# Optimization experiments

Hardware: AMD Instinct MI355X
Metric: run time of the kernel (lower is better)

## Reference

```python
import jax, jax.numpy as jnp
import numpy as np


def setup_inputs() -> dict:
    key = jax.random.key(0)
    ks = jax.random.split(key, 8)
    B, T, U = 4, 400, 80
    De, Dd, V = 512, 512, 1024
    F = De + Dd  # in_features = 1024
    s = lambda k, shape: jax.random.normal(k, shape, dtype=jnp.float32) * 0.05
    return {
        "encoder_output": jax.random.normal(ks[0], (B, T, De), dtype=jnp.float32),
        "decoder_output": jax.random.normal(ks[1], (B, U, Dd), dtype=jnp.float32),
        "W_enc": s(ks[2], (F, De)),
        "b_enc": s(ks[3], (F,)),
        "W_dec": s(ks[4], (F, Dd)),
        "b_dec": s(ks[5], (F,)),
        "W_fc": s(ks[6], (V, F)),
        "b_fc": s(ks[7], (V,)),
    }


def reference(encoder_output, decoder_output, W_enc, b_enc, W_dec, b_dec, W_fc, b_fc):
    # fc_enc / fc_dec projections: (B,T,F) and (B,U,F)
    enc = jnp.einsum("btd,fd->btf", encoder_output, W_enc) + b_enc
    dec = jnp.einsum("bud,fd->buf", decoder_output, W_dec) + b_dec
    # broadcast-add -> (B,T,U,F)
    combined = enc[:, :, None, :] + dec[:, None, :, :]
    # fc: tanh then linear -> (B,T,U,V)
    vocab_logits = jnp.einsum("btuf,vf->btuv", jnp.tanh(combined), W_fc) + b_fc
    # HAT branch: blank prob via sigmoid of logit 0
    blk_logit = vocab_logits[..., :1]
    log_blk = jax.nn.log_sigmoid(blk_logit)          # log(sigmoid)
    log_not_blk = jax.nn.log_sigmoid(-blk_logit)     # log(1 - sigmoid)
    vocab_log_probs = log_not_blk + jax.nn.log_softmax(vocab_logits[..., 1:], axis=-1)
    return jnp.concatenate([log_blk, vocab_log_probs], axis=-1)
```

## Files before the change

kernel.cpp:

```cpp
#include <hip/hip_runtime.h>
#include <hip/hip_bf16.h>
#include <cstdint>
#include <cstddef>

typedef short bf16x8 __attribute__((ext_vector_type(8)));
typedef float f32x4 __attribute__((ext_vector_type(4)));

static __device__ __forceinline__ unsigned short f2bf(float f) {
    union { float f; uint32_t u; } c; c.f = f;
    uint32_t r = c.u + 0x7FFFu + ((c.u >> 16) & 1u);
    return (unsigned short)(r >> 16);
}
static __device__ __forceinline__ float bf2f_lo(uint32_t w) {
    union { uint32_t u; float f; } c; c.u = w << 16; return c.f;
}
static __device__ __forceinline__ float bf2f_hi(uint32_t w) {
    union { uint32_t u; float f; } c; c.u = w & 0xffff0000u; return c.f;
}
static __device__ __forceinline__ float fast_tanh(float x) {
    float e = __expf(2.0f * x);
    return 1.0f - 2.0f / (e + 1.0f);
}
static __device__ __forceinline__ float softplus_f(float x) {
    return fmaxf(x, 0.0f) + log1pf(__expf(-fabsf(x)));
}

#define GLOAD_LDS16(g, l) \
    __builtin_amdgcn_global_load_lds((const __attribute__((address_space(1))) void*)(g), \
                                     (__attribute__((address_space(3))) void*)(l), 16, 0, 0)

__global__ __launch_bounds__(256) void k_convert(
    const float* __restrict__ s0, const float* __restrict__ s1,
    const float* __restrict__ s2, const float* __restrict__ s3,
    const float* __restrict__ s4,
    unsigned short* __restrict__ d0, unsigned short* __restrict__ d1,
    unsigned short* __restrict__ d2, unsigned short* __restrict__ d3,
    unsigned short* __restrict__ d4,
    int n0, int n1, int n2, int n3, int n4)
{
    int i = blockIdx.x * 256 + threadIdx.x;
    int c0 = n0 >> 2, c1 = c0 + (n1 >> 2), c2 = c1 + (n2 >> 2),
        c3 = c2 + (n3 >> 2), c4 = c3 + (n4 >> 2);
    if (i >= c4) return;
    const float* s; unsigned short* d; int j;
    if (i < c0)      { s = s0; d = d0; j = i; }
    else if (i < c1) { s = s1; d = d1; j = i - c0; }
    else if (i < c2) { s = s2; d = d2; j = i - c1; }
    else if (i < c3) { s = s3; d = d3; j = i - c2; }
    else             { s = s4; d = d4; j = i - c3; }
    float4 v = reinterpret_cast<const float4*>(s)[j];
    ushort4 o;
    o.x = f2bf(v.x); o.y = f2bf(v.y); o.z = f2bf(v.z); o.w = f2bf(v.w);
    reinterpret_cast<ushort4*>(d)[j] = o;
}

__global__ __launch_bounds__(256) void k_proj(
    const unsigned short* __restrict__ A,
    const unsigned short* __restrict__ W,
    const float* __restrict__ bias,
    float* __restrict__ out)
{
    __shared__ unsigned short As[32 * 512];
    const int tid = threadIdx.x;
    const int m0 = blockIdx.x * 32;
    const int c0 = blockIdx.y * 128;
    {
        int row = tid >> 3;
        const unsigned short* src = A + (size_t)(m0 + row) * 512;
        unsigned int base = row * 1024;
        unsigned int sw = (row & 7) << 4;
        #pragma unroll
        for (int c = 0; c < 8; ++c) {
            int col = (tid & 7) * 8 + c * 64;
            bf16x8 v = *reinterpret_cast<const bf16x8*>(src + col);
            *reinterpret_cast<bf16x8*>(
                reinterpret_cast<char*>(As) + ((base + col * 2) ^ sw)) = v;
        }
    }
    __syncthreads();
    const int w = tid >> 6, l = tid & 63;
    const int lr = l & 15, lkb = (l >> 4) * 8;
    f32x4 acc[2][2] = {};
    const int colbase = c0 + w * 32;
    const unsigned short* Wb = W + (size_t)(colbase + lr) * 512 + lkb;
    const unsigned int sw = (lr & 7) << 4;
    for (int ks = 0; ks < 16; ++ks) {
        unsigned int kb = (ks * 32 + lkb) * 2;
        bf16x8 a0 = *reinterpret_cast<const bf16x8*>(
            reinterpret_cast<const char*>(As) + ((lr * 1024 + kb) ^ sw));
        bf16x8 a1 = *reinterpret_cast<const bf16x8*>(
            reinterpret_cast<const char*>(As) + (((16 + lr) * 1024 + kb) ^ sw));
        #pragma unroll
        for (int nf = 0; nf < 2; ++nf) {
            bf16x8 b = *reinterpret_cast<const bf16x8*>(Wb + nf * 16 * 512 + ks * 32);
            acc[0][nf] = __builtin_amdgcn_mfma_f32_16x16x32_bf16(a0, b, acc[0][nf], 0, 0, 0);
            acc[1][nf] = __builtin_amdgcn_mfma_f32_16x16x32_bf16(a1, b, acc[1][nf], 0, 0, 0);
        }
    }
    const int qr = (l >> 4) * 4;
    #pragma unroll
    for (int nf = 0; nf < 2; ++nf) {
        int col = colbase + nf * 16 + lr;
        float bv = bias[col];
        #pragma unroll
        for (int mf = 0; mf < 2; ++mf)
            #pragma unroll
            for (int r = 0; r < 4; ++r)
                out[(size_t)(m0 + mf * 16 + qr + r) * 1024 + col] = acc[mf][nf][r] + bv;
    }
}

__global__ __launch_bounds__(256) void k_tanhA(
    const float* __restrict__ enc_f,
    const float* __restrict__ dec_f,
    char* __restrict__ outb)
{
    const int NG = 128000 * 128;
    for (int g = blockIdx.x * 256 + threadIdx.x; g < NG; g += gridDim.x * 256) {
        int row = g >> 7, c8 = g & 127;
        int bt = row / 80;
        int u = row - bt * 80;
        int b = bt / 400;
        const float* ep = enc_f + (size_t)bt * 1024 + c8 * 8;
        const float* dp = dec_f + (size_t)(b * 80 + u) * 1024 + c8 * 8;
        float4 e0 = *(const float4*)ep, e1 = *(const float4*)(ep + 4);
        float4 f0 = *(const float4*)dp, f1 = *(const float4*)(dp + 4);
        uint4 pk;
        pk.x = (uint32_t)f2bf(fast_tanh(e0.x + f0.x)) | ((uint32_t)f2bf(fast_tanh(e0.y + f0.y)) << 16);
        pk.y = (uint32_t)f2bf(fast_tanh(e0.z + f0.z)) | ((uint32_t)f2bf(fast_tanh(e0.w + f0.w)) << 16);
        pk.z = (uint32_t)f2bf(fast_tanh(e1.x + f1.x)) | ((uint32_t)f2bf(fast_tanh(e1.y + f1.y)) << 16);
        pk.w = (uint32_t)f2bf(fast_tanh(e1.z + f1.z)) | ((uint32_t)f2bf(fast_tanh(e1.w + f1.w)) << 16);
        *(uint4*)(outb + (size_t)row * 4096 + c8 * 16) = pk;
    }
}

__global__ __launch_bounds__(512, 1) void k_gemm(
    const unsigned short* __restrict__ Wfc,
    const float* __restrict__ bfc,
    char* __restrict__ outb)
{
    extern __shared__ char smem[];
    const int tid = threadIdx.x;
    const int w = tid >> 6, l = tid & 63;
    const int lr = l & 15, q = l >> 4;
    const int wm = w >> 2, wn = w & 3;

    const int bid = (int)blockIdx.x;
    const int g = (bid & 7) * 250 + (bid >> 3);
    const size_t R0 = (size_t)(g >> 2) * 256;
    const int n0 = (g & 3) * 256;

    const unsigned kb0 = (unsigned)(((tid & 7) * 16) ^ (((tid >> 3) & 7) << 4));
    const int row0 = tid >> 3;
    const char* sA = outb + (R0 + row0) * 4096 + kb0;
    const char* sB = (const char*)Wfc + (size_t)(n0 + row0) * 2048 + kb0;

#define STAGE(dbuf, koff) do { \
    const char* _a = sA + (koff); \
    const char* _b = sB + (koff); \
    char* _d = smem + (dbuf) * 65536 + tid * 16; \
    GLOAD_LDS16(_a,          _d);          \
    GLOAD_LDS16(_a + 262144, _d + 8192);   \
    GLOAD_LDS16(_a + 524288, _d + 16384);  \
    GLOAD_LDS16(_a + 786432, _d + 24576);  \
    GLOAD_LDS16(_b,          _d + 32768);  \
    GLOAD_LDS16(_b + 131072, _d + 40960);  \
    GLOAD_LDS16(_b + 262144, _d + 49152);  \
    GLOAD_LDS16(_b + 393216, _d + 57344);  \
} while (0)

    const unsigned key = (unsigned)((lr & 7) << 4);
    const unsigned kx0 = (unsigned)(q * 16) ^ key;
    const unsigned kx1 = (unsigned)(q * 16 + 64) ^ key;
    const unsigned abase = (unsigned)((wm * 128 + lr) * 128);
    const unsigned bbase = (unsigned)(32768 + (wn * 64 + lr) * 128);

    f32x4 acc[8][4] = {};
    bf16x8 af[4][2], bf[4][2];

    STAGE(0, 0);
    asm volatile("s_waitcnt vmcnt(0)" ::: "memory");
    __builtin_amdgcn_s_barrier();
    __builtin_amdgcn_sched_barrier(0);

#define LDA(h) do { \
    _Pragma("unroll") \
    for (int mf = 0; mf < 4; ++mf) { \
        const char* _p = smem + cb + abase + (h) * 8192 + mf * 2048; \
        af[mf][0] = *(const bf16x8*)(_p + kx0); \
        af[mf][1] = *(const bf16x8*)(_p + kx1); \
    } } while (0)
#define LDB(gg) do { \
    _Pragma("unroll") \
    for (int j = 0; j < 2; ++j) { \
        const char* _p = smem + cb + bbase + ((gg) * 2 + j) * 2048; \
        bf[(gg) * 2 + j][0] = *(const bf16x8*)(_p + kx0); \
        bf[(gg) * 2 + j][1] = *(const bf16x8*)(_p + kx1); \
    } } while (0)
#define MFQ(h, gg) do { \
    __builtin_amdgcn_s_setprio(1); \
    _Pragma("unroll") \
    for (int j = 0; j < 2; ++j) \
        _Pragma("unroll") \
        for (int ks = 0; ks < 2; ++ks) \
            _Pragma("unroll") \
            for (int mf = 0; mf < 4; ++mf) \
                acc[(h) * 4 + mf][(gg) * 2 + j] = __builtin_amdgcn_mfma_f32_16x16x32_bf16( \
                    bf[(gg) * 2 + j][ks], af[mf][ks], acc[(h) * 4 + mf][(gg) * 2 + j], 0, 0, 0); \
    __builtin_amdgcn_s_setprio(0); \
} while (0)

    #pragma unroll 2
    for (int t = 0; t < 16; ++t) {
        const unsigned cb = (unsigned)(t & 1) * 65536;
        if (t + 1 < 16) STAGE((t & 1) ^ 1, (t + 1) * 128);
        LDA(0);
        LDB(0);
        __builtin_amdgcn_s_barrier();
        MFQ(0, 0);
        LDB(1);
        __builtin_amdgcn_s_barrier();
        MFQ(0, 1);
        LDA(1);
        __builtin_amdgcn_s_barrier();
        MFQ(1, 1);
        __builtin_amdgcn_s_barrier();
        MFQ(1, 0);
        asm volatile("s_waitcnt vmcnt(0)" ::: "memory");
        __builtin_amdgcn_s_barrier();
        __builtin_amdgcn_sched_barrier(0);
    }
#undef LDA
#undef LDB
#undef MFQ
#undef STAGE

    #pragma unroll
    for (int nf = 0; nf < 4; ++nf) {
        const int v = n0 + wn * 64 + nf * 16 + q * 4;
        float4 bv = *(const float4*)(bfc + v);
        #pragma unroll
        for (int mf8 = 0; mf8 < 8; ++mf8) {
            f32x4 a = acc[mf8][nf];
            uint2 pk;
            pk.x = (uint32_t)f2bf(a[0] + bv.x) | ((uint32_t)f2bf(a[1] + bv.y) << 16);
            pk.y = (uint32_t)f2bf(a[2] + bv.z) | ((uint32_t)f2bf(a[3] + bv.w) << 16);
            size_t m = R0 + (size_t)(wm * 128 + mf8 * 16 + lr);
            *(uint2*)(outb + m * 4096 + 2048 + (size_t)v * 2) = pk;
        }
    }
}

__global__ __launch_bounds__(256) void k_softmax(char* __restrict__ outb)
{
    const int row = blockIdx.x * 4 + (threadIdx.x >> 6);
    const int l = threadIdx.x & 63;
    const char* lp = outb + (size_t)row * 4096 + 2048 + l * 32;
    uint4 wa = *(const uint4*)lp;
    uint4 wb = *(const uint4*)(lp + 16);
    float v[16];
    uint32_t wd[8] = { wa.x, wa.y, wa.z, wa.w, wb.x, wb.y, wb.z, wb.w };
    #pragma unroll
    for (int i = 0; i < 8; ++i) { v[2*i] = bf2f_lo(wd[i]); v[2*i+1] = bf2f_hi(wd[i]); }

    float l0 = __shfl(v[0], 0);
    float m = (l == 0) ? -3.0e38f : v[0];
    #pragma unroll
    for (int i = 1; i < 16; ++i) m = fmaxf(m, v[i]);
    #pragma unroll
    for (int s = 1; s < 64; s <<= 1) m = fmaxf(m, __shfl_xor(m, s));
    float s = (l == 0) ? 0.0f : __expf(v[0] - m);
    #pragma unroll
    for (int i = 1; i < 16; ++i) s += __expf(v[i] - m);
    #pragma unroll
    for (int sh = 1; sh < 64; sh <<= 1) s += __shfl_xor(s, sh);

    float lse = m + __logf(s);
    float fin = -lse - softplus_f(l0);
    float f0v = -softplus_f(-l0);

    float* op = (float*)(outb + (size_t)row * 4096) + l * 16;
    #pragma unroll
    for (int c = 0; c < 4; ++c) {
        float4 o;
        o.x = v[4*c+0] + fin; o.y = v[4*c+1] + fin;
        o.z = v[4*c+2] + fin; o.w = v[4*c+3] + fin;
        if (l == 0 && c == 0) o.x = f0v;
        *(float4*)(op + 4*c) = o;
    }
}

extern "C" void kernel_launch(void* const* d_in, const int* in_sizes, int n_in,
                              void* d_out, int out_size, void* d_ws, size_t ws_size,
                              hipStream_t stream)
{
    const float* encoder = (const float*)d_in[0];
    const float* decoder = (const float*)d_in[1];
    const float* W_enc   = (const float*)d_in[2];
    const float* b_enc   = (const float*)d_in[3];
    const float* W_dec   = (const float*)d_in[4];
    const float* b_dec   = (const float*)d_in[5];
    const float* W_fc    = (const float*)d_in[6];
    const float* b_fc    = (const float*)d_in[7];
    char* outb = (char*)d_out;

    char* ws = (char*)d_ws;
    float*          enc_f  = (float*)(ws);
    float*          dec_f  = (float*)(ws + 6553600);
    unsigned short* Wfc_h  = (unsigned short*)(ws + 7864320);
    unsigned short* Wenc_h = (unsigned short*)(ws + 9961472);
    unsigned short* Wdec_h = (unsigned short*)(ws + 11010048);
    unsigned short* encI_h = (unsigned short*)(ws + 12058624);
    unsigned short* decI_h = (unsigned short*)(ws + 13697024);

    const int nEnc = 4 * 400 * 512, nDec = 4 * 80 * 512;
    const int nWe = 1024 * 512, nWd = 1024 * 512, nWf = 1024 * 1024;
    const int totalF4 = (nEnc + nDec + nWe + nWd + nWf) >> 2;
    k_convert<<<(totalF4 + 255) / 256, 256, 0, stream>>>(
        encoder, decoder, W_enc, W_dec, W_fc,
        encI_h, decI_h, Wenc_h, Wdec_h, Wfc_h,
        nEnc, nDec, nWe, nWd, nWf);

    k_proj<<<dim3(1600 / 32, 8), 256, 0, stream>>>(encI_h, Wenc_h, b_enc, enc_f);
    k_proj<<<dim3(320 / 32, 8), 256, 0, stream>>>(decI_h, Wdec_h, b_dec, dec_f);

    k_tanhA<<<4096, 256, 0, stream>>>(enc_f, dec_f, outb);

    const int GEMM_SMEM = 131072;
    hipFuncSetAttribute(reinterpret_cast<const void*>(k_gemm),
                        hipFuncAttributeMaxDynamicSharedMemorySize, GEMM_SMEM);
    k_gemm<<<2000, 512, GEMM_SMEM, stream>>>(Wfc_h, b_fc, outb);

    k_softmax<<<32000, 256, 0, stream>>>(outb);
}
```

Baseline: 697.4 us.

## Interleave global-to-LDS prefetch chunks across MFMA phases with deeper lookahead

```diff
diff --git a/kernel.cpp b/kernel.cpp
--- a/kernel.cpp
+++ b/kernel.cpp
@@ -154,11 +154,11 @@
     const int row0 = tid >> 3;
     const char* sA = outb + (R0 + row0) * 4096 + kb0;
     const char* sB = (const char*)Wfc + (size_t)(n0 + row0) * 2048 + kb0;
-
-#define STAGE(dbuf, koff) do { \
-    const char* _a = sA + (koff); \
-    const char* _b = sB + (koff); \
-    char* _d = smem + (dbuf) * 65536 + tid * 16; \
+    char* const dbase = smem + tid * 16;
+
+#define STG_ALL8(buf, T) do { \
+    const char* _a = sA + (T) * 128; const char* _b = sB + (T) * 128; \
+    char* _d = dbase + (buf); \
     GLOAD_LDS16(_a,          _d);          \
     GLOAD_LDS16(_a + 262144, _d + 8192);   \
     GLOAD_LDS16(_a + 524288, _d + 16384);  \
@@ -168,6 +168,14 @@
     GLOAD_LDS16(_b + 262144, _d + 49152);  \
     GLOAD_LDS16(_b + 393216, _d + 57344);  \
 } while (0)
+#define STG_A13(buf, T) do { const char* _a = sA + (T) * 128; char* _d = dbase + (buf); \
+    GLOAD_LDS16(_a + 262144, _d + 8192); GLOAD_LDS16(_a + 786432, _d + 24576); } while (0)
+#define STG_B01(buf, T) do { const char* _b = sB + (T) * 128; char* _d = dbase + (buf); \
+    GLOAD_LDS16(_b,          _d + 32768); GLOAD_LDS16(_b + 131072, _d + 40960); } while (0)
+#define STG_B23(buf, T) do { const char* _b = sB + (T) * 128; char* _d = dbase + (buf); \
+    GLOAD_LDS16(_b + 262144, _d + 49152); GLOAD_LDS16(_b + 393216, _d + 57344); } while (0)
+#define STG_A02(buf, T) do { const char* _a = sA + (T) * 128; char* _d = dbase + (buf); \
+    GLOAD_LDS16(_a,          _d);         GLOAD_LDS16(_a + 524288, _d + 16384); } while (0)
 
     const unsigned key = (unsigned)((lr & 7) << 4);
     const unsigned kx0 = (unsigned)(q * 16) ^ key;
@@ -177,11 +185,6 @@
 
     f32x4 acc[8][4] = {};
     bf16x8 af[4][2], bf[4][2];
-
-    STAGE(0, 0);
-    asm volatile("s_waitcnt vmcnt(0)" ::: "memory");
-    __builtin_amdgcn_s_barrier();
-    __builtin_amdgcn_sched_barrier(0);
 
 #define LDA(h) do { \
     _Pragma("unroll") \
@@ -209,31 +212,53 @@
                     bf[(gg) * 2 + j][ks], af[mf][ks], acc[(h) * 4 + mf][(gg) * 2 + j], 0, 0, 0); \
     __builtin_amdgcn_s_setprio(0); \
 } while (0)
+#define BAR __builtin_amdgcn_s_barrier()
+
+    STG_ALL8(0u, 0);
+    STG_A02(65536u, 1);
+    asm volatile("s_waitcnt vmcnt(2)" ::: "memory");
+    BAR;
+    __builtin_amdgcn_sched_barrier(0);
 
     #pragma unroll 2
     for (int t = 0; t < 16; ++t) {
-        const unsigned cb = (unsigned)(t & 1) * 65536;
-        if (t + 1 < 16) STAGE((t & 1) ^ 1, (t + 1) * 128);
-        LDA(0);
-        LDB(0);
-        __builtin_amdgcn_s_barrier();
+        const unsigned cb = (unsigned)(t & 1) * 65536u;
+        const unsigned nb = cb ^ 65536u;
+        const bool s1 = (t + 1 < 16), s2 = (t + 2 < 16);
+        LDA(0); LDB(0);
+        if (s1) STG_A13(nb, t + 1);
+        BAR;
         MFQ(0, 0);
         LDB(1);
-        __builtin_amdgcn_s_barrier();
+        if (s1) STG_B01(nb, t + 1);
+        BAR;
         MFQ(0, 1);
         LDA(1);
-        __builtin_amdgcn_s_barrier();
+        if (s1) STG_B23(nb, t + 1);
+        BAR;
         MFQ(1, 1);
-        __builtin_amdgcn_s_barrier();
+        if (s2) STG_A02(cb, t + 2);
+        BAR;
         MFQ(1, 0);
-        asm volatile("s_waitcnt vmcnt(0)" ::: "memory");
-        __builtin_amdgcn_s_barrier();
-        __builtin_amdgcn_sched_barrier(0);
+        if (t < 14) {
+            asm volatile("s_waitcnt vmcnt(2)" ::: "memory");
+            BAR;
+            __builtin_amdgcn_sched_barrier(0);
+        } else if (t == 14) {
+            asm volatile("s_waitcnt vmcnt(0)" ::: "memory");
+            BAR;
+            __builtin_amdgcn_sched_barrier(0);
+        }
     }
 #undef LDA
 #undef LDB
 #undef MFQ
-#undef STAGE
+#undef BAR
+#undef STG_ALL8
+#undef STG_A13
+#undef STG_B01
+#undef STG_B23
+#undef STG_A02
 
     #pragma unroll
     for (int nf = 0; nf < 4; ++nf) {
```

Measured after the change: 655.5 us. -6.0%, faster.
